# Optimization experiments

Hardware: AMD Instinct MI355X
Metric: run time of the kernel (lower is better)

## Reference

```python
import jax, jax.numpy as jnp
import numpy as np

HID, NH, NKV, HD, INTER = 2560, 8, 4, 256, 10240
WIN, EPS, BASE = 512, 1e-6, 10000.0
B, S = 1, 2048


def rmsnorm(x, w, eps=EPS):
    # Gemma-style: fp32 norm, scale by (1 + weight)
    x32 = x.astype(jnp.float32)
    n = x32 * jax.lax.rsqrt(jnp.mean(x32 * x32, axis=-1, keepdims=True) + eps)
    return (n * (1.0 + w.astype(jnp.float32))).astype(x.dtype)


def rotate_half(x):
    x1, x2 = jnp.split(x, 2, axis=-1)
    return jnp.concatenate([-x2, x1], axis=-1)


def rope_cos_sin(position_ids, dim=HD, base=BASE):
    inv_freq = 1.0 / (base ** (jnp.arange(0, dim, 2, dtype=jnp.float32) / dim))
    freqs = position_ids.astype(jnp.float32)[..., None] * inv_freq  # [B,S,D/2]
    emb = jnp.concatenate([freqs, freqs], axis=-1)  # [B,S,D]
    return jnp.cos(emb), jnp.sin(emb)


def setup_inputs() -> dict:
    key = jax.random.key(0)
    ks = jax.random.split(key, 16)
    s = 0.02
    return {
        "hidden_states": jax.random.normal(ks[0], (B, S, HID), jnp.float32),
        "position_ids": jnp.broadcast_to(jnp.arange(S, dtype=jnp.int32)[None, :], (B, S)),
        "wq": jax.random.normal(ks[1], (HID, NH * HD), jnp.float32) * s,
        "wk": jax.random.normal(ks[2], (HID, NKV * HD), jnp.float32) * s,
        "wv": jax.random.normal(ks[3], (HID, NKV * HD), jnp.float32) * s,
        "wo": jax.random.normal(ks[4], (NH * HD, HID), jnp.float32) * s,
        "q_ln_w": jax.random.normal(ks[5], (HD,), jnp.float32) * s,
        "k_ln_w": jax.random.normal(ks[6], (HD,), jnp.float32) * s,
        "in_ln_w": jax.random.normal(ks[7], (HID,), jnp.float32) * s,
        "post_attn_ln_w": jax.random.normal(ks[8], (HID,), jnp.float32) * s,
        "pre_ff_ln_w": jax.random.normal(ks[9], (HID,), jnp.float32) * s,
        "post_ff_ln_w": jax.random.normal(ks[10], (HID,), jnp.float32) * s,
        "w_gate": jax.random.normal(ks[11], (HID, INTER), jnp.float32) * s,
        "w_up": jax.random.normal(ks[12], (HID, INTER), jnp.float32) * s,
        "w_down": jax.random.normal(ks[13], (INTER, HID), jnp.float32) * s,
    }


def reference(hidden_states, position_ids, wq, wk, wv, wo, q_ln_w, k_ln_w,
              in_ln_w, post_attn_ln_w, pre_ff_ln_w, post_ff_ln_w,
              w_gate, w_up, w_down):
    x = hidden_states
    residual = x
    h = rmsnorm(x, in_ln_w)

    # --- attention (GQA, per-head QK RMSNorm, rotary, sliding-window) ---
    bsz, q_len, _ = h.shape
    Q = (h @ wq).reshape(bsz, q_len, NH, HD).transpose(0, 2, 1, 3)   # [B,H,S,D]
    K = (h @ wk).reshape(bsz, q_len, NKV, HD).transpose(0, 2, 1, 3)  # [B,Hkv,S,D]
    V = (h @ wv).reshape(bsz, q_len, NKV, HD).transpose(0, 2, 1, 3)

    Q = rmsnorm(Q, q_ln_w)
    K = rmsnorm(K, k_ln_w)

    cos, sin = rope_cos_sin(position_ids)            # [B,S,D]
    cos, sin = cos[:, None], sin[:, None]            # [B,1,S,D]
    Q = Q * cos + rotate_half(Q) * sin
    K = K * cos + rotate_half(K) * sin

    groups = NH // NKV
    K = jnp.repeat(K, groups, axis=1)  # [B,H,S,D]
    V = jnp.repeat(V, groups, axis=1)

    scale = math_sqrt_hd = HD ** 0.5
    scores = jnp.einsum("bhqd,bhkd->bhqk", Q, K) / scale

    i = jnp.arange(q_len)[:, None]
    j = jnp.arange(q_len)[None, :]
    mask = (j <= i) & (i - j < WIN)  # [S,S]
    neg = jnp.finfo(scores.dtype).min
    scores = jnp.where(mask[None, None], scores, neg)

    probs = jax.nn.softmax(scores.astype(jnp.float32), axis=-1).astype(Q.dtype)
    attn = jnp.einsum("bhqk,bhkd->bhqd", probs, V)   # [B,H,S,D]
    attn = attn.transpose(0, 2, 1, 3).reshape(bsz, q_len, NH * HD)
    attn = attn @ wo

    attn = rmsnorm(attn, post_attn_ln_w)
    x = residual + attn

    # --- MLP (gated gelu-tanh) ---
    residual = x
    h = rmsnorm(x, pre_ff_ln_w)
    mlp = (jax.nn.gelu(h @ w_gate, approximate=True) * (h @ w_up)) @ w_down
    mlp = rmsnorm(mlp, post_ff_ln_w)
    return residual + mlp
```

## Files before the change

### kernel.cpp

```cpp
#include <hip/hip_runtime.h>


using u16 = unsigned short;
using u32 = unsigned int;
using short8  = __attribute__((ext_vector_type(8))) short;
using floatx4 = __attribute__((ext_vector_type(4))) float;

__device__ __forceinline__ float bf2f(u16 u) { return __uint_as_float(((u32)u) << 16); }
__device__ __forceinline__ u16 f2bf(float f) {
  u32 b = __float_as_uint(f);
  return (u16)((b + 0x7fffu + ((b >> 16) & 1u)) >> 16);
}
__device__ __forceinline__ float ldf(const float* p) { return *p; }
__device__ __forceinline__ float ldf(const u16* p) { return bf2f(*p); }
__device__ __forceinline__ void stf(float* p, float v) { *p = v; }
__device__ __forceinline__ void stf(u16* p, float v) { *p = f2bf(v); }
__device__ __forceinline__ float gelu_tanh(float x) {
  float u = 0.7978845608028654f * (x + 0.044715f * x * x * x);
  return 0.5f * x * (1.f + tanhf(u));
}
__device__ __forceinline__ void async16(const u16* g, u16* l) {
  __builtin_amdgcn_global_load_lds((const __attribute__((address_space(1))) void*)g,
                                   (__attribute__((address_space(3))) void*)l, 16, 0, 0);
}
#define MFMA(a, b, c) __builtin_amdgcn_mfma_f32_16x16x32_bf16((a), (b), (c), 0, 0, 0)

__global__ __launch_bounds__(256) void transpose_f2b_k(const float* __restrict__ src,
                                                       u16* __restrict__ dst,
                                                       int ss, int ds) {
  __shared__ u16 tile[128][66];
  const int t  = threadIdx.y * 64 + threadIdx.x;
  const int r0 = blockIdx.y * 64;
  const int c0 = blockIdx.x * 128;
#pragma unroll
  for (int i = 0; i < 16; ++i) {
    int u = i * 256 + t;
    int r = u >> 6;
    int cu = u & 63;
    float2 v = *(const float2*)(src + (size_t)(r0 + r) * ss + c0 + cu * 2);
    tile[cu * 2][r]     = f2bf(v.x);
    tile[cu * 2 + 1][r] = f2bf(v.y);
  }
  __syncthreads();
#pragma unroll
  for (int i = 0; i < 16; ++i) {
    int u = i * 256 + t;
    int c = u >> 5;
    int ru = u & 31;
    u32 v = (u32)tile[c][ru * 2] | ((u32)tile[c][ru * 2 + 1] << 16);
    *(u32*)(dst + (size_t)(c0 + c) * ds + r0 + ru * 2) = v;
  }
}

__global__ __launch_bounds__(256) void transpose_b2b_k(const u16* __restrict__ src,
                                                       u16* __restrict__ dst,
                                                       int ss, int ds) {
  __shared__ u16 tile[128][66];
  const int t  = threadIdx.y * 64 + threadIdx.x;
  const int r0 = blockIdx.y * 64;
  const int c0 = blockIdx.x * 128;
#pragma unroll
  for (int i = 0; i < 16; ++i) {
    int u = i * 256 + t;
    int r = u >> 6;
    int cu = u & 63;
    u32 v = *(const u32*)(src + (size_t)(r0 + r) * ss + c0 + cu * 2);
    tile[cu * 2][r]     = (u16)v;
    tile[cu * 2 + 1][r] = (u16)(v >> 16);
  }
  __syncthreads();
#pragma unroll
  for (int i = 0; i < 16; ++i) {
    int u = i * 256 + t;
    int c = u >> 5;
    int ru = u & 31;
    u32 v = (u32)tile[c][ru * 2] | ((u32)tile[c][ru * 2 + 1] << 16);
    *(u32*)(dst + (size_t)(c0 + c) * ds + r0 + ru * 2) = v;
  }
}

template <typename TI, typename TO, bool RES>
__global__ __launch_bounds__(256) void rmsnorm_k(const TI* __restrict__ in,
                                                 const float* __restrict__ w,
                                                 const float* __restrict__ res,
                                                 TO* __restrict__ out) {
  const int row = blockIdx.x, t = threadIdx.x;
  const TI* ip = in + (size_t)row * 2560;
  float v[10];
  float ss = 0.f;
#pragma unroll
  for (int i = 0; i < 10; ++i) {
    v[i] = ldf(ip + t + i * 256);
    ss += v[i] * v[i];
  }
#pragma unroll
  for (int o = 32; o; o >>= 1) ss += __shfl_xor(ss, o, 64);
  __shared__ float ws4[4];
  if ((t & 63) == 0) ws4[t >> 6] = ss;
  __syncthreads();
  ss = (ws4[0] + ws4[1] + ws4[2] + ws4[3]) * (1.f / 2560.f);
  const float inv = rsqrtf(ss + 1e-6f);
#pragma unroll
  for (int i = 0; i < 10; ++i) {
    int c = t + i * 256;
    float o = v[i] * inv * (1.f + w[c]);
    if (RES) o += res[(size_t)row * 2560 + c];
    stf(out + (size_t)row * 2560 + c, o);
  }
}

__global__ __launch_bounds__(256) void qkrope_k(u16* __restrict__ qkv,
                                                const float* __restrict__ qw,
                                                const float* __restrict__ kw,
                                                const int* __restrict__ pos) {
  const int s = blockIdx.y, j = blockIdx.x, d = threadIdx.x;
  const int col = (j < 8) ? j * 256 : 2048 + (j - 8) * 256;
  const float* w = (j < 8) ? qw : kw;
  u16* p = qkv + (size_t)s * 4096 + col;
  float x = bf2f(p[d]);
  float ss = x * x;
#pragma unroll
  for (int o = 32; o; o >>= 1) ss += __shfl_xor(ss, o, 64);
  __shared__ float ws4[4];
  __shared__ float nb[256];
  if ((d & 63) == 0) ws4[d >> 6] = ss;
  __syncthreads();
  ss = (ws4[0] + ws4[1] + ws4[2] + ws4[3]) * (1.f / 256.f);
  float n = x * rsqrtf(ss + 1e-6f) * (1.f + w[d]);
  nb[d] = n;
  __syncthreads();
  float partner = nb[d ^ 128];
  float rot = (d < 128) ? -partner : partner;
  float ang = (float)pos[s] * exp2f((float)(d & 127) * (-13.287712379549449f / 128.f));
  float sn, cs;
  sincosf(ang, &sn, &cs);
  p[d] = f2bf(n * cs + rot * sn);
}

template <int EPI>
__global__ __launch_bounds__(256, 2) void gemm_bt(const u16* __restrict__ A,
                                                  const u16* __restrict__ B,
                                                  u16* __restrict__ C,
                                                  const u16* __restrict__ Up,
                                                  int M, int N, int K) {
  __shared__ u16 lA[128 * 32];
  __shared__ u16 lB[128 * 32];
  const int t = threadIdx.x;
  const int wave = t >> 6, lane = t & 63;
  const int quad = lane >> 4, lq = lane & 15;
  const int wm = wave >> 1, wn = wave & 1;
  const int bm = blockIdx.y * 128, bn = blockIdx.x * 128;

  floatx4 acc[4][4];
#pragma unroll
  for (int i = 0; i < 4; ++i)
#pragma unroll
    for (int j = 0; j < 4; ++j) acc[i][j] = (floatx4){0.f, 0.f, 0.f, 0.f};

  const u16* ga = A + (size_t)(bm + (t >> 2)) * K + (t & 3) * 8;
  const u16* gb = B + (size_t)(bn + (t >> 2)) * K + (t & 3) * 8;
  u16* la = lA + t * 8;
  u16* lb = lB + t * 8;
  const int halfs = 64 * K;

  for (int k0 = 0; k0 < K; k0 += 32) {
    async16(ga + k0, la);
    async16(ga + k0 + halfs, la + 2048);
    async16(gb + k0, lb);
    async16(gb + k0 + halfs, lb + 2048);
    __syncthreads();
    short8 af[4], bf[4];
#pragma unroll
    for (int i = 0; i < 4; ++i)
      af[i] = *(const short8*)(lA + (wm * 64 + i * 16 + lq) * 32 + quad * 8);
#pragma unroll
    for (int j = 0; j < 4; ++j)
      bf[j] = *(const short8*)(lB + (wn * 64 + j * 16 + lq) * 32 + quad * 8);
#pragma unroll
    for (int i = 0; i < 4; ++i)
#pragma unroll
      for (int j = 0; j < 4; ++j) acc[i][j] = MFMA(af[i], bf[j], acc[i][j]);
    __syncthreads();
  }
#pragma unroll
  for (int i = 0; i < 4; ++i) {
    const int row = bm + wm * 64 + i * 16 + quad * 4;
#pragma unroll
    for (int j = 0; j < 4; ++j) {
      const int col = bn + wn * 64 + j * 16 + lq;
#pragma unroll
      for (int r = 0; r < 4; ++r) {
        float v = acc[i][j][r];
        size_t idx = (size_t)(row + r) * N + col;
        if (EPI == 1) v = gelu_tanh(v) * bf2f(Up[idx]);
        C[idx] = f2bf(v);
      }
    }
  }
}

__global__ __launch_bounds__(256, 2) void attn_k(const u16* __restrict__ qkv,
                                                 const u16* __restrict__ vT,
                                                 u16* __restrict__ out) {
  __shared__ u16 pb[4][16 * 32];
  const int t = threadIdx.x;
  const int wave = t >> 6, lane = t & 63;
  const int quad = lane >> 4, lq = lane & 15;
  const int h = blockIdx.y, kvh = h >> 1;
  const int q0 = (blockIdx.x * 4 + wave) * 16;

  short8 qf[8];
  {
    const u16* qb = qkv + (size_t)(q0 + lq) * 4096 + h * 256 + quad * 8;
#pragma unroll
    for (int kk = 0; kk < 8; ++kk) qf[kk] = *(const short8*)(qb + kk * 32);
  }
  floatx4 acc[16];
#pragma unroll
  for (int n = 0; n < 16; ++n) acc[n] = (floatx4){0.f, 0.f, 0.f, 0.f};
  float mrun[4] = {-1e30f, -1e30f, -1e30f, -1e30f};
  float lrun[4] = {0.f, 0.f, 0.f, 0.f};

  int kstart = q0 - (512 - 1);
  if (kstart < 0) kstart = 0;
  kstart &= ~31;
  const int kend = q0 + 15;
  const u16* kb = qkv + 2048 + (size_t)kvh * 256 + quad * 8;
  const u16* vb = vT + (size_t)(kvh * 256 + lq) * 2048 + quad * 8;
  u16* pw = pb[wave];

  for (int kt = kstart; kt <= kend; kt += 32) {
    short8 kf[16];
#pragma unroll
    for (int hlf = 0; hlf < 2; ++hlf)
#pragma unroll
      for (int kk = 0; kk < 8; ++kk)
        kf[hlf * 8 + kk] =
            *(const short8*)(kb + (size_t)(kt + hlf * 16 + lq) * 4096 + kk * 32);
    floatx4 s0 = (floatx4){0.f, 0.f, 0.f, 0.f};
    floatx4 s1 = s0;
#pragma unroll
    for (int kk = 0; kk < 8; ++kk) {
      s0 = MFMA(qf[kk], kf[kk], s0);
      s1 = MFMA(qf[kk], kf[8 + kk], s1);
    }
#pragma unroll
    for (int r = 0; r < 4; ++r) {
      const int q = q0 + quad * 4 + r;
      const int k0i = kt + lq, k1i = k0i + 16;
      float sc0 = s0[r] * 0.0625f, sc1 = s1[r] * 0.0625f;
      const bool m0 = (k0i <= q) && (q - k0i < 512);
      const bool m1 = (k1i <= q) && (q - k1i < 512);
      sc0 = m0 ? sc0 : -1e30f;
      sc1 = m1 ? sc1 : -1e30f;
      float mx = fmaxf(sc0, sc1);
#pragma unroll
      for (int o = 8; o; o >>= 1) mx = fmaxf(mx, __shfl_xor(mx, o, 64));
      const float mn = fmaxf(mrun[r], mx);
      const float al = __expf(mrun[r] - mn);
      const float p0 = m0 ? __expf(sc0 - mn) : 0.f;
      const float p1 = m1 ? __expf(sc1 - mn) : 0.f;
      float rs = p0 + p1;
#pragma unroll
      for (int o = 8; o; o >>= 1) rs += __shfl_xor(rs, o, 64);
      lrun[r] = lrun[r] * al + rs;
      mrun[r] = mn;
#pragma unroll
      for (int n = 0; n < 16; ++n) acc[n][r] *= al;
      pw[(quad * 4 + r) * 32 + lq] = f2bf(p0);
      pw[(quad * 4 + r) * 32 + 16 + lq] = f2bf(p1);
    }
    __asm__ volatile("s_waitcnt lgkmcnt(0)" ::: "memory");
    const short8 pa = *(const short8*)(pw + lq * 32 + quad * 8);
#pragma unroll
    for (int n = 0; n < 16; ++n) {
      const short8 vf = *(const short8*)(vb + (size_t)(n * 16) * 2048 + kt);
      acc[n] = MFMA(pa, vf, acc[n]);
    }
  }
#pragma unroll
  for (int n = 0; n < 16; ++n)
#pragma unroll
    for (int r = 0; r < 4; ++r) {
      const int q = q0 + quad * 4 + r;
      out[(size_t)q * 2048 + h * 256 + n * 16 + lq] = f2bf(acc[n][r] / lrun[r]);
    }
}

extern "C" void kernel_launch(void* const* d_in, const int* in_sizes, int n_in,
                              void* d_out, int out_size, void* d_ws, size_t ws_size,
                              hipStream_t stream) {
  (void)in_sizes; (void)n_in; (void)out_size; (void)ws_size;
  const float* x    = (const float*)d_in[0];
  const int*   pos  = (const int*)d_in[1];
  const float* wq   = (const float*)d_in[2];
  const float* wk   = (const float*)d_in[3];
  const float* wv   = (const float*)d_in[4];
  const float* wo   = (const float*)d_in[5];
  const float* qlw  = (const float*)d_in[6];
  const float* klw  = (const float*)d_in[7];
  const float* inln = (const float*)d_in[8];
  const float* paln = (const float*)d_in[9];
  const float* pfln = (const float*)d_in[10];
  const float* poln = (const float*)d_in[11];
  const float* wg   = (const float*)d_in[12];
  const float* wu   = (const float*)d_in[13];
  const float* wd   = (const float*)d_in[14];

  u16* ws    = (u16*)d_ws;
  u16* qkvT  = ws;
  u16* woT   = qkvT + 10485760;
  u16* wgT   = woT + 5242880;
  u16* wuT   = wgT + 26214400;
  u16* wdT   = wuT + 26214400;
  u16* h1    = wdT + 26214400;
  u16* qkv   = h1 + 5242880;
  u16* vT    = qkv + 8388608;
  u16* attno = vT + 2097152;
  u16* up    = attno + 4194304;
  float* x2  = (float*)qkvT;
  u16* h2    = qkv;

  const dim3 tb(64, 4);
  transpose_f2b_k<<<dim3(2048 / 128, 2560 / 64), tb, 0, stream>>>(wq, qkvT, 2048, 2560);
  transpose_f2b_k<<<dim3(1024 / 128, 2560 / 64), tb, 0, stream>>>(wk, qkvT + (size_t)2048 * 2560, 1024, 2560);
  transpose_f2b_k<<<dim3(1024 / 128, 2560 / 64), tb, 0, stream>>>(wv, qkvT + (size_t)3072 * 2560, 1024, 2560);
  transpose_f2b_k<<<dim3(2560 / 128, 2048 / 64), tb, 0, stream>>>(wo, woT, 2560, 2048);
  transpose_f2b_k<<<dim3(10240 / 128, 2560 / 64), tb, 0, stream>>>(wg, wgT, 10240, 2560);
  transpose_f2b_k<<<dim3(10240 / 128, 2560 / 64), tb, 0, stream>>>(wu, wuT, 10240, 2560);
  transpose_f2b_k<<<dim3(2560 / 128, 10240 / 64), tb, 0, stream>>>(wd, wdT, 2560, 10240);

  rmsnorm_k<float, u16, false><<<2048, 256, 0, stream>>>(x, inln, nullptr, h1);
  gemm_bt<0><<<dim3(4096 / 128, 2048 / 128), 256, 0, stream>>>(h1, qkvT, qkv, nullptr, 2048, 4096, 2560);
  qkrope_k<<<dim3(12, 2048), 256, 0, stream>>>(qkv, qlw, klw, pos);
  transpose_b2b_k<<<dim3(1024 / 128, 2048 / 64), tb, 0, stream>>>(qkv + 3072, vT, 4096, 2048);
  attn_k<<<dim3(2048 / 64, 8), 256, 0, stream>>>(qkv, vT, attno);
  gemm_bt<0><<<dim3(2560 / 128, 2048 / 128), 256, 0, stream>>>(attno, woT, h1, nullptr, 2048, 2560, 2048);
  rmsnorm_k<u16, float, true><<<2048, 256, 0, stream>>>(h1, paln, x, x2);
  rmsnorm_k<float, u16, false><<<2048, 256, 0, stream>>>(x2, pfln, nullptr, h2);
  gemm_bt<0><<<dim3(10240 / 128, 2048 / 128), 256, 0, stream>>>(h2, wuT, up, nullptr, 2048, 10240, 2560);
  gemm_bt<1><<<dim3(10240 / 128, 2048 / 128), 256, 0, stream>>>(h2, wgT, wuT, up, 2048, 10240, 2560);
  gemm_bt<0><<<dim3(2560 / 128, 2048 / 128), 256, 0, stream>>>(wuT, wdT, woT, nullptr, 2048, 2560, 10240);
  rmsnorm_k<u16, float, true><<<2048, 256, 0, stream>>>(woT, poln, x2, (float*)d_out);
}
```

Before: 1.190 ms.

## Double-buffer GEMM LDS tiles, raise occupancy hint, and use exp-based tanh in GELU

The bf16 GEMM now keeps two LDS buffers for the A and B tiles. It issues the async global-to-LDS loads for the next K step before the MFMAs on the current one, and drops to a single barrier per iteration, so memory latency can overlap with compute. The launch-bounds occupancy hint goes from 2 to 3 blocks per CU, which caps registers per thread more tightly and risks spills. GELU's tanhf is replaced with a formula built on __expf, trading a little accuracy for cheaper math in the gate epilogue.

```diff
diff --git a/kernel.cpp b/kernel.cpp
--- a/kernel.cpp
+++ b/kernel.cpp
@@ -17,7 +17,9 @@
 __device__ __forceinline__ void stf(u16* p, float v) { *p = f2bf(v); }
 __device__ __forceinline__ float gelu_tanh(float x) {
   float u = 0.7978845608028654f * (x + 0.044715f * x * x * x);
-  return 0.5f * x * (1.f + tanhf(u));
+  float t = __expf(2.f * u);
+  float th = 1.f - 2.f / (t + 1.f);
+  return 0.5f * x * (1.f + th);
 }
 __device__ __forceinline__ void async16(const u16* g, u16* l) {
   __builtin_amdgcn_global_load_lds((const __attribute__((address_space(1))) void*)g,
@@ -138,13 +140,13 @@
 }
 
 template <int EPI>
-__global__ __launch_bounds__(256, 2) void gemm_bt(const u16* __restrict__ A,
+__global__ __launch_bounds__(256, 3) void gemm_bt(const u16* __restrict__ A,
                                                   const u16* __restrict__ B,
                                                   u16* __restrict__ C,
                                                   const u16* __restrict__ Up,
                                                   int M, int N, int K) {
-  __shared__ u16 lA[128 * 32];
-  __shared__ u16 lB[128 * 32];
+  __shared__ u16 lA[2][128 * 32];
+  __shared__ u16 lB[2][128 * 32];
   const int t = threadIdx.x;
   const int wave = t >> 6, lane = t & 63;
   const int quad = lane >> 4, lq = lane & 15;
@@ -159,28 +161,39 @@
 
   const u16* ga = A + (size_t)(bm + (t >> 2)) * K + (t & 3) * 8;
   const u16* gb = B + (size_t)(bn + (t >> 2)) * K + (t & 3) * 8;
-  u16* la = lA + t * 8;
-  u16* lb = lB + t * 8;
   const int halfs = 64 * K;
-
-  for (int k0 = 0; k0 < K; k0 += 32) {
-    async16(ga + k0, la);
-    async16(ga + k0 + halfs, la + 2048);
-    async16(gb + k0, lb);
-    async16(gb + k0 + halfs, lb + 2048);
+  const int toff = t * 8;
+
+  async16(ga, lA[0] + toff);
+  async16(ga + halfs, lA[0] + 2048 + toff);
+  async16(gb, lB[0] + toff);
+  async16(gb + halfs, lB[0] + 2048 + toff);
+
+  const int niter = K >> 5;
+  for (int i = 0; i < niter; ++i) {
     __syncthreads();
+    if (i + 1 < niter) {
+      const int k0 = (i + 1) << 5;
+      u16* lan = lA[(i + 1) & 1];
+      u16* lbn = lB[(i + 1) & 1];
+      async16(ga + k0, lan + toff);
+      async16(ga + k0 + halfs, lan + 2048 + toff);
+      async16(gb + k0, lbn + toff);
+      async16(gb + k0 + halfs, lbn + 2048 + toff);
+    }
+    const u16* la = lA[i & 1];
+    const u16* lb = lB[i & 1];
     short8 af[4], bf[4];
 #pragma unroll
-    for (int i = 0; i < 4; ++i)
-      af[i] = *(const short8*)(lA + (wm * 64 + i * 16 + lq) * 32 + quad * 8);
+    for (int ii = 0; ii < 4; ++ii)
+      af[ii] = *(const short8*)(la + (wm * 64 + ii * 16 + lq) * 32 + quad * 8);
 #pragma unroll
     for (int j = 0; j < 4; ++j)
-      bf[j] = *(const short8*)(lB + (wn * 64 + j * 16 + lq) * 32 + quad * 8);
-#pragma unroll
-    for (int i = 0; i < 4; ++i)
-#pragma unroll
-      for (int j = 0; j < 4; ++j) acc[i][j] = MFMA(af[i], bf[j], acc[i][j]);
-    __syncthreads();
+      bf[j] = *(const short8*)(lb + (wn * 64 + j * 16 + lq) * 32 + quad * 8);
+#pragma unroll
+    for (int ii = 0; ii < 4; ++ii)
+#pragma unroll
+      for (int j = 0; j < 4; ++j) acc[ii][j] = MFMA(af[ii], bf[j], acc[ii][j]);
   }
 #pragma unroll
   for (int i = 0; i < 4; ++i) {
```

Result: faster. 1.156 ms (-2.9%).
